# Performance work log

Hardware: AMD Instinct MI355X
Metric: run time of the kernel (lower is better)

The kernel has to match this reference:

```python
import jax, jax.numpy as jnp
import numpy as np
import math

B, S = 2, 2048                      # batch, seq_len (equal-length varlen pack)
NUM_HEADS, HEAD_DIM = 32, 128
NUM_KV_HEADS = 8                    # GQA group size = 4
WINDOW = 1024                       # sliding window (window_size, 0)
SCALE = 1.0 / math.sqrt(HEAD_DIM)


def get_slopes(n):
    # n=32 is a power of two -> simple geometric slopes (matches torch get_slopes)
    start = 2.0 ** (-2.0 ** (-(math.log2(n) - 3)))
    return np.array([start * start ** i for i in range(n)], dtype=np.float32)


def setup_inputs() -> dict:
    key = jax.random.key(0)
    kq, kk, kv = jax.random.split(key, 3)
    q = jax.random.normal(kq, (B * S, NUM_HEADS * HEAD_DIM), dtype=jnp.float32)
    k = jax.random.normal(kk, (B * S, NUM_KV_HEADS * HEAD_DIM), dtype=jnp.float32)
    v = jax.random.normal(kv, (B * S, NUM_KV_HEADS * HEAD_DIM), dtype=jnp.float32)
    return {"q": q, "k": k, "v": v}


def reference(q, k, v):
    # Prefill self-attention path of Attention.forward:
    # flash_attn_varlen_func(q, k, v, causal=True, window_size=(WINDOW, 0),
    #                        alibi_slopes=get_slopes(num_heads), softmax_scale=SCALE)
    slopes = jnp.asarray(get_slopes(NUM_HEADS))               # [H]
    qh = q.reshape(B, S, NUM_HEADS, HEAD_DIM)                 # [B,S,H,D]
    g = NUM_HEADS // NUM_KV_HEADS
    kh = jnp.repeat(k.reshape(B, S, NUM_KV_HEADS, HEAD_DIM), g, axis=2)
    vh = jnp.repeat(v.reshape(B, S, NUM_KV_HEADS, HEAD_DIM), g, axis=2)

    scores = jnp.einsum('bihd,bjhd->bhij', qh, kh) * SCALE    # [B,H,S,S]
    i = jnp.arange(S)[:, None]
    j = jnp.arange(S)[None, :]
    mask = (j <= i) & (j >= i - WINDOW)                       # causal + sliding window
    alibi = -slopes[:, None, None] * (i - j).astype(jnp.float32)  # [H,S,S]
    neg_inf = jnp.asarray(-jnp.inf, dtype=scores.dtype)
    scores = jnp.where(mask[None, None], scores + alibi[None], neg_inf)
    p = jax.nn.softmax(scores, axis=-1)
    o = jnp.einsum('bhij,bjhd->bihd', p, vh)                  # [B,S,H,D]
    return o.reshape(B * S, NUM_HEADS * HEAD_DIM)
```

## Files before the change

### kernel.cpp

```cpp
#include <hip/hip_runtime.h>
#include <stdint.h>

#define NB 2
#define NS 2048
#define NH 32
#define NKV 8
#define ND 128
#define NWIN 1024
#define KVB 32
#define SCALE2 (0.08838834764831845f * 1.4426950408889634f)
#define LOG2E 1.4426950408889634f

typedef __bf16 bf16x8 __attribute__((ext_vector_type(8)));
typedef float f32x4 __attribute__((ext_vector_type(4)));
typedef unsigned short u16x4 __attribute__((ext_vector_type(4)));
typedef unsigned short u16x8 __attribute__((ext_vector_type(8)));
typedef unsigned int u32x2 __attribute__((ext_vector_type(2)));

union Frag { u16x8 u; bf16x8 b; u32x2 w[2]; __bf16 e[8]; };
union BF4 { u16x4 u; __bf16 b[4]; };
union BF8 { u16x8 u; __bf16 b[8]; };

__device__ __forceinline__ void gload16(const unsigned short* g, unsigned short* l) {
  __builtin_amdgcn_global_load_lds(
      (const __attribute__((address_space(1))) unsigned int*)g,
      (__attribute__((address_space(3))) unsigned int*)l, 16, 0, 0);
}

__global__ __launch_bounds__(256)
void cvt_kv(const float* __restrict__ k, const float* __restrict__ v,
            unsigned short* __restrict__ kbf, unsigned short* __restrict__ vbf) {
  const int i = blockIdx.x * blockDim.x + threadIdx.x;
  float4 a0 = ((const float4*)k)[i * 2], a1 = ((const float4*)k)[i * 2 + 1];
  float4 b0 = ((const float4*)v)[i * 2], b1 = ((const float4*)v)[i * 2 + 1];
  BF8 ko, vo;
  ko.b[0] = (__bf16)a0.x; ko.b[1] = (__bf16)a0.y; ko.b[2] = (__bf16)a0.z; ko.b[3] = (__bf16)a0.w;
  ko.b[4] = (__bf16)a1.x; ko.b[5] = (__bf16)a1.y; ko.b[6] = (__bf16)a1.z; ko.b[7] = (__bf16)a1.w;
  vo.b[0] = (__bf16)b0.x; vo.b[1] = (__bf16)b0.y; vo.b[2] = (__bf16)b0.z; vo.b[3] = (__bf16)b0.w;
  vo.b[4] = (__bf16)b1.x; vo.b[5] = (__bf16)b1.y; vo.b[6] = (__bf16)b1.z; vo.b[7] = (__bf16)b1.w;
  ((u16x8*)kbf)[i] = ko.u;
  ((u16x8*)vbf)[i] = vo.u;
}

__global__ __launch_bounds__(256)
void attn_gqa(const unsigned short* __restrict__ kbf,
              const unsigned short* __restrict__ vbf,
              const float* __restrict__ qg, float* __restrict__ og) {
  __shared__ unsigned short k_lds[3][KVB * 128];
  __shared__ unsigned short v_lds[3][KVB * 128];

  const int tid = threadIdx.x;
  const int w = tid >> 6;
  const int lane = tid & 63;
  const int l15 = lane & 15;
  const int lg = lane >> 4;

  const int bid = blockIdx.x;
  const int hkv = bid & 7;
  const int rest = bid >> 3;
  const int b = (rest >= 48) ? 1 : 0;
  const int slot = rest - b * 48;
  const int h = hkv * 4 + w;
  const float slope2 = exp2f(-0.25f * (float)(h + 1)) * LOG2E;

  int koff_e[2], voff_e[2];
#pragma unroll
  for (int i = 0; i < 2; ++i) {
    const int rk = (w * 2 + i) * 4 + lg;
    const int c = l15;
    const int sig = ((rk >> 2) & 3) * 8 + ((rk >> 4) & 1) * 4 + (rk & 3);
    koff_e[i] = sig * (NKV * ND) + ((c ^ (rk & 7)) * 8);
    const int e0 = (w * 2 + i) * 512 + lane * 8;
    const int sx0 = e0 & 15;
    const int vj = (e0 >> 4) & 3;
    const int vg_ = (e0 >> 6) & 3;
    const int s1 = (e0 >> 8) & 1;
    const int scv = (e0 >> 9) & 7;
    voff_e[i] = (vg_ * 8 + s1 * 4 + vj) * (NKV * ND) + scv * 16 + sx0;
  }
  const unsigned short* kpan = kbf + (size_t)b * NS * (NKV * ND) + hkv * ND;
  const unsigned short* vpan = vbf + (size_t)b * NS * (NKV * ND) + hkv * ND;

  auto stage = [&](int t, int buf) {
    const size_t eb = (size_t)(t * KVB) * (NKV * ND);
#pragma unroll
    for (int i = 0; i < 2; ++i) {
      gload16(kpan + eb + koff_e[i], &k_lds[buf][(w * 2 + i) * 512]);
      gload16(vpan + eb + voff_e[i], &v_lds[buf][(w * 2 + i) * 512]);
    }
  };

  auto run_band = [&](int q0) {
    const int qiA = q0 + l15;
    const int qiB = qiA + 16;

    u16x8 qfA[4], qfB[4];
#pragma unroll
    for (int half = 0; half < 2; ++half) {
      const int qi = half ? qiB : qiA;
      const float* qp = qg + (size_t)(b * NS + qi) * (NH * ND) + h * ND;
#pragma unroll
      for (int ks = 0; ks < 4; ++ks) {
        const int dbase = ks * 32 + lg * 8;
        float4 f0 = *(const float4*)(qp + dbase);
        float4 f1 = *(const float4*)(qp + dbase + 4);
        Frag q_;
        q_.e[0] = (__bf16)f0.x; q_.e[1] = (__bf16)f0.y;
        q_.e[2] = (__bf16)f0.z; q_.e[3] = (__bf16)f0.w;
        q_.e[4] = (__bf16)f1.x; q_.e[5] = (__bf16)f1.y;
        q_.e[6] = (__bf16)f1.z; q_.e[7] = (__bf16)f1.w;
        if (half) qfB[ks] = q_.u; else qfA[ks] = q_.u;
      }
    }

    float mA = 0.f, lA = 0.f, mB = 0.f, lB = 0.f;
    f32x4 accA[8], accB[8];
#pragma unroll
    for (int c = 0; c < 8; ++c) {
      accA[c][0] = 0.f; accA[c][1] = 0.f; accA[c][2] = 0.f; accA[c][3] = 0.f;
      accB[c][0] = 0.f; accB[c][1] = 0.f; accB[c][2] = 0.f; accB[c][3] = 0.f;
    }

    const int t0 = (q0 >= NWIN) ? ((q0 - NWIN) >> 5) : 0;
    const int t1 = q0 >> 5;

    stage(t1, 0);
    if (t1 - 1 >= t0) stage(t1 - 1, 1);

    int idx = 0;
    for (int t = t1; t >= t0; --t, ++idx) {
      const int kvbase = t * KVB;
      if (t > t0) asm volatile("s_waitcnt vmcnt(4)" ::: "memory");
      else        asm volatile("s_waitcnt vmcnt(0)" ::: "memory");
      __builtin_amdgcn_s_barrier();
      if (t - 2 >= t0) stage(t - 2, (idx + 2) % 3);
      const int cur = idx % 3;

      const bool interior = (kvbase + 31 <= q0) && (kvbase >= q0 + 31 - NWIN);

      f32x4 sA[2], sB[2];
#pragma unroll
      for (int f = 0; f < 2; ++f) {
        sA[f][0] = 0.f; sA[f][1] = 0.f; sA[f][2] = 0.f; sA[f][3] = 0.f;
        sB[f][0] = 0.f; sB[f][1] = 0.f; sB[f][2] = 0.f; sB[f][3] = 0.f;
      }
      const int xo = (l15 & 7) << 4;
      __builtin_amdgcn_s_setprio(1);
#pragma unroll
      for (int ks = 0; ks < 4; ++ks) {
        const int db2 = ks * 64 + lg * 16;
        Frag qa, qb;
        qa.u = qfA[ks]; qb.u = qfB[ks];
#pragma unroll
        for (int f = 0; f < 2; ++f) {
          Frag kb;
          kb.u = *(const u16x8*)((const char*)&k_lds[cur][0] +
                                 (((f * 16 + l15) * 256 + db2) ^ xo));
          sA[f] = __builtin_amdgcn_mfma_f32_16x16x32_bf16(kb.b, qa.b, sA[f], 0, 0, 0);
          sB[f] = __builtin_amdgcn_mfma_f32_16x16x32_bf16(kb.b, qb.b, sB[f], 0, 0, 0);
        }
      }
      __builtin_amdgcn_s_setprio(0);

      Frag pbA, pbB;
      auto softmax_half = [&](const f32x4* s, int dbse, float& m_r, float& l_r,
                              f32x4* acc, Frag& pb) {
        float x[2][4];
        if (interior) {
          const float ab2 = fmaf(-slope2, (float)dbse, -m_r);
#pragma unroll
          for (int f = 0; f < 2; ++f)
#pragma unroll
            for (int r = 0; r < 4; ++r)
              x[f][r] = fmaf(s[f][r], SCALE2,
                             fmaf(slope2, (float)(f * 4 + r), ab2));
        } else {
#pragma unroll
          for (int f = 0; f < 2; ++f)
#pragma unroll
            for (int r = 0; r < 4; ++r) {
              const int d = dbse - (f * 4 + r);
              const float val = fmaf(s[f][r], SCALE2, -slope2 * (float)d) - m_r;
              x[f][r] = ((unsigned)d <= (unsigned)NWIN) ? val : -1e30f;
            }
        }
        float tm = fmaxf(fmaxf(fmaxf(x[0][0], x[0][1]), x[0][2]),
                         fmaxf(fmaxf(x[0][3], x[1][0]), x[1][1]));
        tm = fmaxf(tm, fmaxf(x[1][2], x[1][3]));
        if (!__all(tm <= 8.0f)) {
          tm = fmaxf(tm, __shfl_xor(tm, 16, 64));
          tm = fmaxf(tm, __shfl_xor(tm, 32, 64));
          const float delta = fmaxf(tm, 0.f);
          const float fac = __builtin_amdgcn_exp2f(-delta);
          m_r += delta;
          l_r *= fac;
#pragma unroll
          for (int c = 0; c < 8; ++c) acc[c] = acc[c] * fac;
#pragma unroll
          for (int f = 0; f < 2; ++f)
#pragma unroll
            for (int r = 0; r < 4; ++r) x[f][r] -= delta;
        }
        float e[8];
#pragma unroll
        for (int f = 0; f < 2; ++f)
#pragma unroll
          for (int r = 0; r < 4; ++r) {
            e[f * 4 + r] = __builtin_amdgcn_exp2f(x[f][r]);
            pb.e[f * 4 + r] = (__bf16)e[f * 4 + r];
          }
        l_r += ((e[0] + e[1]) + (e[2] + e[3])) + ((e[4] + e[5]) + (e[6] + e[7]));
      };
      softmax_half(sA, qiA - kvbase - lg * 8, mA, lA, accA, pbA);
      softmax_half(sB, qiB - kvbase - lg * 8, mB, lB, accB, pbB);

      Frag vb4[4];
      const unsigned int vbase = (unsigned int)(uintptr_t)(&v_lds[cur][0]) + lane * 8;
#pragma unroll
      for (int cp = 0; cp < 4; ++cp) {
        const unsigned int a = vbase + cp * 1024;
        asm volatile("ds_read_b64_tr_b16 %0, %1" : "=v"(vb4[cp].w[0]) : "v"(a));
        asm volatile("ds_read_b64_tr_b16 %0, %1 offset:512" : "=v"(vb4[cp].w[1]) : "v"(a));
      }
      __builtin_amdgcn_s_setprio(1);
#pragma unroll
      for (int c = 0; c < 8; ++c) {
        if (c == 5)      asm volatile("s_waitcnt lgkmcnt(4)" ::: "memory");
        else if (c == 6) asm volatile("s_waitcnt lgkmcnt(2)" ::: "memory");
        else if (c == 7) asm volatile("s_waitcnt lgkmcnt(0)" ::: "memory");
        else             asm volatile("s_waitcnt lgkmcnt(6)" ::: "memory");
        __builtin_amdgcn_sched_barrier(0);
        accA[c] = __builtin_amdgcn_mfma_f32_16x16x32_bf16(vb4[c & 3].b, pbA.b, accA[c], 0, 0, 0);
        accB[c] = __builtin_amdgcn_mfma_f32_16x16x32_bf16(vb4[c & 3].b, pbB.b, accB[c], 0, 0, 0);
        if (c < 4) {
          const unsigned int a2 = vbase + (c + 4) * 1024;
          asm volatile("ds_read_b64_tr_b16 %0, %1" : "=v"(vb4[c].w[0]) : "v"(a2));
          asm volatile("ds_read_b64_tr_b16 %0, %1 offset:512" : "=v"(vb4[c].w[1]) : "v"(a2));
        }
      }
      __builtin_amdgcn_s_setprio(0);
      __builtin_amdgcn_sched_barrier(0);
    }

    lA += __shfl_xor(lA, 16, 64);
    lA += __shfl_xor(lA, 32, 64);
    lB += __shfl_xor(lB, 16, 64);
    lB += __shfl_xor(lB, 32, 64);
    {
      const float inv = 1.0f / lA;
      float* op = og + (size_t)(b * NS + qiA) * (NH * ND) + h * ND + lg * 4;
#pragma unroll
      for (int c = 0; c < 8; ++c) { f32x4 o = accA[c] * inv; *(f32x4*)(op + c * 16) = o; }
    }
    {
      const float inv = 1.0f / lB;
      float* op = og + (size_t)(b * NS + qiB) * (NH * ND) + h * ND + lg * 4;
#pragma unroll
      for (int c = 0; c < 8; ++c) { f32x4 o = accB[c] * inv; *(f32x4*)(op + c * 16) = o; }
    }
    __builtin_amdgcn_s_barrier();
  };

  if (slot < 32) {
    run_band((slot + 32) * 32);
  } else {
    const int s = slot - 32;
    run_band(s * 32);
    run_band((31 - s) * 32);
  }
}

__global__ __launch_bounds__(256, 2)
void attn_fb(const float* __restrict__ qg, const float* __restrict__ kg,
             const float* __restrict__ vg, float* __restrict__ og) {
  __shared__ unsigned short k_lds[64 * 128];
  __shared__ unsigned short v_lds[64 * 128];
  const int tid = threadIdx.x;
  const int w = tid >> 6;
  const int lane = tid & 63;
  const int l15 = lane & 15;
  const int lg = lane >> 4;
  const int bid = blockIdx.x;
  const int h = bid & 31;
  const int qt = 31 - ((bid >> 5) & 31);
  const int b = bid >> 10;
  const int hkv = h >> 2;
  const float slope2 = exp2f(-0.25f * (float)(h + 1)) * LOG2E;
  const int q0 = qt * 64;
  const int qi = q0 + w * 16 + l15;
  u16x8 qf[4];
  {
    const float* qp = qg + (size_t)(b * NS + qi) * (NH * ND) + h * ND;
#pragma unroll
    for (int ks = 0; ks < 4; ++ks) {
      const int dbase = ks * 32 + lg * 8;
      float4 f0 = *(const float4*)(qp + dbase);
      float4 f1 = *(const float4*)(qp + dbase + 4);
      Frag q_;
      q_.e[0] = (__bf16)f0.x; q_.e[1] = (__bf16)f0.y;
      q_.e[2] = (__bf16)f0.z; q_.e[3] = (__bf16)f0.w;
      q_.e[4] = (__bf16)f1.x; q_.e[5] = (__bf16)f1.y;
      q_.e[6] = (__bf16)f1.z; q_.e[7] = (__bf16)f1.w;
      qf[ks] = q_.u;
    }
  }
  float m_r = -1e30f, l_r = 0.f;
  f32x4 acc[8];
#pragma unroll
  for (int c = 0; c < 8; ++c) { acc[c][0] = 0.f; acc[c][1] = 0.f; acc[c][2] = 0.f; acc[c][3] = 0.f; }
  const int srow = tid >> 5;
  const int sdb = (tid & 31) * 4;
  const int sc = sdb >> 4;
  const int sx = sdb & 15;
  float4 kreg[8], vreg[8];
  const int t0 = (q0 >= NWIN) ? ((q0 - NWIN) >> 6) : 0;
  const int t1 = q0 >> 6;
  auto load_tile = [&](int t) {
    const int kvbase = t * 64;
#pragma unroll
    for (int it = 0; it < 8; ++it) {
      const size_t go = (size_t)(b * NS + kvbase + it * 8 + srow) * (NKV * ND) + hkv * ND + sdb;
      kreg[it] = *(const float4*)(kg + go);
      vreg[it] = *(const float4*)(vg + go);
    }
  };
  load_tile(t0);
  for (int t = t0; t <= t1; ++t) {
    const int kvbase = t * 64;
    __syncthreads();
#pragma unroll
    for (int it = 0; it < 8; ++it) {
      const int row = it * 8 + srow;
      BF4 ku, vu;
      ku.b[0] = (__bf16)kreg[it].x; ku.b[1] = (__bf16)kreg[it].y;
      ku.b[2] = (__bf16)kreg[it].z; ku.b[3] = (__bf16)kreg[it].w;
      vu.b[0] = (__bf16)vreg[it].x; vu.b[1] = (__bf16)vreg[it].y;
      vu.b[2] = (__bf16)vreg[it].z; vu.b[3] = (__bf16)vreg[it].w;
      const int rk = ((row & 4) << 3) | ((row & 56) >> 1) | (row & 3);
      const int kb = (rk * 256 + sdb * 2) ^ ((rk & 7) << 4);
      *(u16x4*)((char*)k_lds + kb) = ku.u;
      const int s2 = ((row >> 5) << 1) | ((row >> 2) & 1);
      const int vi = sc * 1024 + s2 * 256 + ((row >> 3) & 3) * 64 + (row & 3) * 16 + sx;
      *(u16x4*)(&v_lds[vi]) = vu.u;
    }
    __syncthreads();
    if (t < t1) load_tile(t + 1);
    f32x4 s[4];
#pragma unroll
    for (int f = 0; f < 4; ++f) { s[f][0] = 0.f; s[f][1] = 0.f; s[f][2] = 0.f; s[f][3] = 0.f; }
    const int xo = (l15 & 7) << 4;
#pragma unroll
    for (int ks = 0; ks < 4; ++ks) {
      const int db2 = ks * 64 + lg * 16;
      Frag qa; qa.u = qf[ks];
#pragma unroll
      for (int f = 0; f < 4; ++f) {
        Frag kb;
        kb.u = *(u16x8*)((char*)k_lds + (((f * 16 + l15) * 256 + db2) ^ xo));
        s[f] = __builtin_amdgcn_mfma_f32_16x16x32_bf16(kb.b, qa.b, s[f], 0, 0, 0);
      }
    }
    const int dbse = qi - kvbase - lg * 8;
    float sv[4][4];
#pragma unroll
    for (int f = 0; f < 4; ++f) {
#pragma unroll
      for (int r = 0; r < 4; ++r) {
        const int koff = ((f & 1) << 5) + ((f >> 1) << 2) + r;
        const int d = dbse - koff;
        const float val = fmaf(s[f][r], SCALE2, -slope2 * (float)d);
        sv[f][r] = ((unsigned)d <= (unsigned)NWIN) ? val : -1e30f;
      }
    }
    float tm = fmaxf(fmaxf(sv[0][0], sv[0][1]), fmaxf(sv[0][2], sv[0][3]));
#pragma unroll
    for (int f = 1; f < 4; ++f)
      tm = fmaxf(tm, fmaxf(fmaxf(sv[f][0], sv[f][1]), fmaxf(sv[f][2], sv[f][3])));
    tm = fmaxf(tm, __shfl_xor(tm, 16, 64));
    tm = fmaxf(tm, __shfl_xor(tm, 32, 64));
    const float newm = fmaxf(m_r, tm);
    const float fac = __builtin_amdgcn_exp2f(m_r - newm);
    m_r = newm;
    float rs = 0.f;
    Frag pb0, pb1;
#pragma unroll
    for (int f = 0; f < 4; ++f) {
      float e0 = __builtin_amdgcn_exp2f(sv[f][0] - m_r);
      float e1 = __builtin_amdgcn_exp2f(sv[f][1] - m_r);
      float e2 = __builtin_amdgcn_exp2f(sv[f][2] - m_r);
      float e3 = __builtin_amdgcn_exp2f(sv[f][3] - m_r);
      rs += (e0 + e1) + (e2 + e3);
      const int base = (f >> 1) * 4;
      if (f & 1) {
        pb1.e[base + 0] = (__bf16)e0; pb1.e[base + 1] = (__bf16)e1;
        pb1.e[base + 2] = (__bf16)e2; pb1.e[base + 3] = (__bf16)e3;
      } else {
        pb0.e[base + 0] = (__bf16)e0; pb0.e[base + 1] = (__bf16)e1;
        pb0.e[base + 2] = (__bf16)e2; pb0.e[base + 3] = (__bf16)e3;
      }
    }
    rs += __shfl_xor(rs, 16, 64);
    rs += __shfl_xor(rs, 32, 64);
    l_r = l_r * fac + rs;
#pragma unroll
    for (int c = 0; c < 8; ++c) acc[c] = acc[c] * fac;
    const unsigned int vbase = (unsigned int)(uintptr_t)(&v_lds[0]) + lane * 8;
#pragma unroll
    for (int c = 0; c < 8; ++c) {
      u32x2 r0, r1, r2, r3;
      const unsigned int a = vbase + c * 2048;
      asm volatile("ds_read_b64_tr_b16 %0, %1" : "=v"(r0) : "v"(a));
      asm volatile("ds_read_b64_tr_b16 %0, %1 offset:512" : "=v"(r1) : "v"(a));
      asm volatile("ds_read_b64_tr_b16 %0, %1 offset:1024" : "=v"(r2) : "v"(a));
      asm volatile("ds_read_b64_tr_b16 %0, %1 offset:1536" : "=v"(r3) : "v"(a));
      asm volatile("s_waitcnt lgkmcnt(0)" ::: "memory");
      __builtin_amdgcn_sched_barrier(0);
      Frag vb0, vb1;
      vb0.w[0] = r0; vb0.w[1] = r1;
      vb1.w[0] = r2; vb1.w[1] = r3;
      acc[c] = __builtin_amdgcn_mfma_f32_16x16x32_bf16(vb0.b, pb0.b, acc[c], 0, 0, 0);
      acc[c] = __builtin_amdgcn_mfma_f32_16x16x32_bf16(vb1.b, pb1.b, acc[c], 0, 0, 0);
    }
  }
  const float inv = 1.0f / l_r;
  float* op = og + (size_t)(b * NS + qi) * (NH * ND) + h * ND + lg * 4;
#pragma unroll
  for (int c = 0; c < 8; ++c) { f32x4 o = acc[c] * inv; *(f32x4*)(op + c * 16) = o; }
}

extern "C" void kernel_launch(void* const* d_in, const int* in_sizes, int n_in,
                              void* d_out, int out_size, void* d_ws, size_t ws_size,
                              hipStream_t stream) {
  (void)in_sizes; (void)n_in; (void)out_size;
  const float* q = (const float*)d_in[0];
  const float* k = (const float*)d_in[1];
  const float* v = (const float*)d_in[2];
  float* out = (float*)d_out;
  const size_t kv_elems = (size_t)NB * NS * NKV * ND;
  const size_t need = 2 * kv_elems * sizeof(unsigned short);
  if (ws_size >= need) {
    unsigned short* kbf = (unsigned short*)d_ws;
    unsigned short* vbf = kbf + kv_elems;
    cvt_kv<<<dim3((unsigned)(kv_elems / 8 / 256)), dim3(256), 0, stream>>>(k, v, kbf, vbf);
    attn_gqa<<<dim3(NB * NKV * 48), dim3(256), 0, stream>>>(kbf, vbf, q, out);
  } else {
    attn_fb<<<dim3(NB * NH * (NS / 64)), dim3(256), 0, stream>>>(q, k, v, out);
  }
}
```

Measured before the change: 122.2 us.

## Replace LDS-staged GQA attention with direct-from-global loads and pre-transposed V

The LDS-staged, barrier-synchronised GQA kernel is replaced. In the old kernel four query heads shared a KV panel through a triple-buffered LDS pipeline. In the new one each wave handles one (batch, head, 32-query tile) independently and loads K and V fragments straight from global memory. A separate preprocessing kernel transposes V into a d-major bf16 layout so the PV MFMA operands can be read as contiguous 16-byte loads. This removes LDS traffic and barriers, at the cost of losing cross-head KV sharing and any async prefetch overlap, and adds an extra launch. The per-block work split also changes from paired causal bands to one wave per tile, with the largest tiles scheduled first.

New measurement: 218.7 us. 79.0% more time.

```diff
diff --git a/kernel.cpp b/kernel.cpp
--- a/kernel.cpp
+++ b/kernel.cpp
@@ -21,252 +21,219 @@
 union BF4 { u16x4 u; __bf16 b[4]; };
 union BF8 { u16x8 u; __bf16 b[8]; };
 
-__device__ __forceinline__ void gload16(const unsigned short* g, unsigned short* l) {
-  __builtin_amdgcn_global_load_lds(
-      (const __attribute__((address_space(1))) unsigned int*)g,
-      (__attribute__((address_space(3))) unsigned int*)l, 16, 0, 0);
+__device__ __forceinline__ unsigned short f2b(float x) {
+  union { __bf16 b; unsigned short u; } c; c.b = (__bf16)x; return c.u;
 }
 
 __global__ __launch_bounds__(256)
-void cvt_kv(const float* __restrict__ k, const float* __restrict__ v,
-            unsigned short* __restrict__ kbf, unsigned short* __restrict__ vbf) {
+void cvt_k(const float* __restrict__ k, unsigned short* __restrict__ kbf) {
   const int i = blockIdx.x * blockDim.x + threadIdx.x;
   float4 a0 = ((const float4*)k)[i * 2], a1 = ((const float4*)k)[i * 2 + 1];
-  float4 b0 = ((const float4*)v)[i * 2], b1 = ((const float4*)v)[i * 2 + 1];
-  BF8 ko, vo;
+  BF8 ko;
   ko.b[0] = (__bf16)a0.x; ko.b[1] = (__bf16)a0.y; ko.b[2] = (__bf16)a0.z; ko.b[3] = (__bf16)a0.w;
   ko.b[4] = (__bf16)a1.x; ko.b[5] = (__bf16)a1.y; ko.b[6] = (__bf16)a1.z; ko.b[7] = (__bf16)a1.w;
-  vo.b[0] = (__bf16)b0.x; vo.b[1] = (__bf16)b0.y; vo.b[2] = (__bf16)b0.z; vo.b[3] = (__bf16)b0.w;
-  vo.b[4] = (__bf16)b1.x; vo.b[5] = (__bf16)b1.y; vo.b[6] = (__bf16)b1.z; vo.b[7] = (__bf16)b1.w;
   ((u16x8*)kbf)[i] = ko.u;
-  ((u16x8*)vbf)[i] = vo.u;
 }
 
 __global__ __launch_bounds__(256)
-void attn_gqa(const unsigned short* __restrict__ kbf,
-              const unsigned short* __restrict__ vbf,
-              const float* __restrict__ qg, float* __restrict__ og) {
-  __shared__ unsigned short k_lds[3][KVB * 128];
-  __shared__ unsigned short v_lds[3][KVB * 128];
-
+void vt_cvt(const float* __restrict__ v, unsigned short* __restrict__ vt) {
+  __shared__ unsigned short lt[128][72];
+  const int bid = blockIdx.x;
+  const int kt = bid & 31;
+  const int hkv = (bid >> 5) & 7;
+  const int b = bid >> 8;
+  const int t = threadIdx.x;
+  const int r = t >> 2;
+  const int dc = (t & 3) * 32;
+  const float* src = v + (size_t)(b * NS + kt * 64 + r) * (NKV * ND) + hkv * ND + dc;
+#pragma unroll
+  for (int j = 0; j < 8; ++j) {
+    float4 x = *(const float4*)(src + j * 4);
+    lt[dc + j * 4 + 0][r] = f2b(x.x);
+    lt[dc + j * 4 + 1][r] = f2b(x.y);
+    lt[dc + j * 4 + 2][r] = f2b(x.z);
+    lt[dc + j * 4 + 3][r] = f2b(x.w);
+  }
+  __syncthreads();
+  const int d = t >> 1;
+  const int kc = (t & 1) * 32;
+  unsigned short* dst = vt + (size_t)((b * NKV + hkv) * ND + d) * NS + kt * 64 + kc;
+#pragma unroll
+  for (int j2 = 0; j2 < 4; ++j2) {
+    u16x8 o;
+#pragma unroll
+    for (int e = 0; e < 8; ++e) o[e] = lt[d][kc + j2 * 8 + e];
+    *(u16x8*)(dst + j2 * 8) = o;
+  }
+}
+
+__global__ __launch_bounds__(256)
+void attn_nl(const unsigned short* __restrict__ kbf,
+             const unsigned short* __restrict__ vt,
+             const float* __restrict__ qg, float* __restrict__ og) {
   const int tid = threadIdx.x;
   const int w = tid >> 6;
   const int lane = tid & 63;
   const int l15 = lane & 15;
   const int lg = lane >> 4;
 
-  const int bid = blockIdx.x;
-  const int hkv = bid & 7;
-  const int rest = bid >> 3;
-  const int b = (rest >= 48) ? 1 : 0;
-  const int slot = rest - b * 48;
-  const int h = hkv * 4 + w;
+  const int u = blockIdx.x * 4 + w;
+  const int qt = 63 - (u >> 6);
+  const int hb = u & 63;
+  const int b = hb >> 5;
+  const int h = hb & 31;
+  const int hkv = h >> 2;
   const float slope2 = exp2f(-0.25f * (float)(h + 1)) * LOG2E;
-
-  int koff_e[2], voff_e[2];
-#pragma unroll
-  for (int i = 0; i < 2; ++i) {
-    const int rk = (w * 2 + i) * 4 + lg;
-    const int c = l15;
-    const int sig = ((rk >> 2) & 3) * 8 + ((rk >> 4) & 1) * 4 + (rk & 3);
-    koff_e[i] = sig * (NKV * ND) + ((c ^ (rk & 7)) * 8);
-    const int e0 = (w * 2 + i) * 512 + lane * 8;
-    const int sx0 = e0 & 15;
-    const int vj = (e0 >> 4) & 3;
-    const int vg_ = (e0 >> 6) & 3;
-    const int s1 = (e0 >> 8) & 1;
-    const int scv = (e0 >> 9) & 7;
-    voff_e[i] = (vg_ * 8 + s1 * 4 + vj) * (NKV * ND) + scv * 16 + sx0;
-  }
+  const int q0 = qt * 32;
+  const int qiA = q0 + l15;
+  const int qiB = qiA + 16;
+
+  u16x8 qfA[4], qfB[4];
+#pragma unroll
+  for (int half = 0; half < 2; ++half) {
+    const int qi = half ? qiB : qiA;
+    const float* qp = qg + (size_t)(b * NS + qi) * (NH * ND) + h * ND;
+#pragma unroll
+    for (int ks = 0; ks < 4; ++ks) {
+      const int dbase = ks * 32 + lg * 8;
+      float4 f0 = *(const float4*)(qp + dbase);
+      float4 f1 = *(const float4*)(qp + dbase + 4);
+      Frag q_;
+      q_.e[0] = (__bf16)f0.x; q_.e[1] = (__bf16)f0.y;
+      q_.e[2] = (__bf16)f0.z; q_.e[3] = (__bf16)f0.w;
+      q_.e[4] = (__bf16)f1.x; q_.e[5] = (__bf16)f1.y;
+      q_.e[6] = (__bf16)f1.z; q_.e[7] = (__bf16)f1.w;
+      if (half) qfB[ks] = q_.u; else qfA[ks] = q_.u;
+    }
+  }
+
   const unsigned short* kpan = kbf + (size_t)b * NS * (NKV * ND) + hkv * ND;
-  const unsigned short* vpan = vbf + (size_t)b * NS * (NKV * ND) + hkv * ND;
-
-  auto stage = [&](int t, int buf) {
-    const size_t eb = (size_t)(t * KVB) * (NKV * ND);
-#pragma unroll
-    for (int i = 0; i < 2; ++i) {
-      gload16(kpan + eb + koff_e[i], &k_lds[buf][(w * 2 + i) * 512]);
-      gload16(vpan + eb + voff_e[i], &v_lds[buf][(w * 2 + i) * 512]);
-    }
-  };
-
-  auto run_band = [&](int q0) {
-    const int qiA = q0 + l15;
-    const int qiB = qiA + 16;
-
-    u16x8 qfA[4], qfB[4];
-#pragma unroll
-    for (int half = 0; half < 2; ++half) {
-      const int qi = half ? qiB : qiA;
-      const float* qp = qg + (size_t)(b * NS + qi) * (NH * ND) + h * ND;
-#pragma unroll
-      for (int ks = 0; ks < 4; ++ks) {
-        const int dbase = ks * 32 + lg * 8;
-        float4 f0 = *(const float4*)(qp + dbase);
-        float4 f1 = *(const float4*)(qp + dbase + 4);
-        Frag q_;
-        q_.e[0] = (__bf16)f0.x; q_.e[1] = (__bf16)f0.y;
-        q_.e[2] = (__bf16)f0.z; q_.e[3] = (__bf16)f0.w;
-        q_.e[4] = (__bf16)f1.x; q_.e[5] = (__bf16)f1.y;
-        q_.e[6] = (__bf16)f1.z; q_.e[7] = (__bf16)f1.w;
-        if (half) qfB[ks] = q_.u; else qfA[ks] = q_.u;
+  const unsigned short* vpan = vt + (size_t)(b * NKV + hkv) * ND * NS;
+  const int sig0 = ((l15 >> 2) << 3) + (l15 & 3);
+
+  float mA = 0.f, lA = 0.f, mB = 0.f, lB = 0.f;
+  f32x4 accA[8], accB[8];
+#pragma unroll
+  for (int c = 0; c < 8; ++c) {
+    accA[c][0] = 0.f; accA[c][1] = 0.f; accA[c][2] = 0.f; accA[c][3] = 0.f;
+    accB[c][0] = 0.f; accB[c][1] = 0.f; accB[c][2] = 0.f; accB[c][3] = 0.f;
+  }
+
+  const int t0 = (q0 >= NWIN) ? ((q0 - NWIN) >> 5) : 0;
+  const int t1 = q0 >> 5;
+
+  for (int t = t1; t >= t0; --t) {
+    const int kvbase = t * KVB;
+    const bool interior = (kvbase + 31 <= q0) && (kvbase >= q0 + 31 - NWIN);
+
+    const unsigned short* k0 = kpan + (size_t)(kvbase + sig0) * (NKV * ND) + lg * 8;
+    const unsigned short* k1 = k0 + 4 * (NKV * ND);
+    Frag kf0[4], kf1[4];
+#pragma unroll
+    for (int ks = 0; ks < 4; ++ks) {
+      kf0[ks].u = *(const u16x8*)(k0 + ks * 32);
+      kf1[ks].u = *(const u16x8*)(k1 + ks * 32);
+    }
+
+    f32x4 sA[2], sB[2];
+#pragma unroll
+    for (int f = 0; f < 2; ++f) {
+      sA[f][0] = 0.f; sA[f][1] = 0.f; sA[f][2] = 0.f; sA[f][3] = 0.f;
+      sB[f][0] = 0.f; sB[f][1] = 0.f; sB[f][2] = 0.f; sB[f][3] = 0.f;
+    }
+    __builtin_amdgcn_s_setprio(1);
+#pragma unroll
+    for (int ks = 0; ks < 4; ++ks) {
+      Frag qa, qb;
+      qa.u = qfA[ks]; qb.u = qfB[ks];
+      sA[0] = __builtin_amdgcn_mfma_f32_16x16x32_bf16(kf0[ks].b, qa.b, sA[0], 0, 0, 0);
+      sB[0] = __builtin_amdgcn_mfma_f32_16x16x32_bf16(kf0[ks].b, qb.b, sB[0], 0, 0, 0);
+      sA[1] = __builtin_amdgcn_mfma_f32_16x16x32_bf16(kf1[ks].b, qa.b, sA[1], 0, 0, 0);
+      sB[1] = __builtin_amdgcn_mfma_f32_16x16x32_bf16(kf1[ks].b, qb.b, sB[1], 0, 0, 0);
+    }
+    __builtin_amdgcn_s_setprio(0);
+
+    Frag vf[8];
+#pragma unroll
+    for (int c = 0; c < 8; ++c)
+      vf[c].u = *(const u16x8*)(vpan + (size_t)(c * 16 + l15) * NS + kvbase + lg * 8);
+
+    Frag pbA, pbB;
+    auto softmax_half = [&](const f32x4* s, int dbse, float& m_r, float& l_r,
+                            f32x4* acc, Frag& pb) {
+      float x[2][4];
+      if (interior) {
+        const float ab2 = fmaf(-slope2, (float)dbse, -m_r);
+#pragma unroll
+        for (int f = 0; f < 2; ++f)
+#pragma unroll
+          for (int r = 0; r < 4; ++r)
+            x[f][r] = fmaf(s[f][r], SCALE2,
+                           fmaf(slope2, (float)(f * 4 + r), ab2));
+      } else {
+#pragma unroll
+        for (int f = 0; f < 2; ++f)
+#pragma unroll
+          for (int r = 0; r < 4; ++r) {
+            const int d = dbse - (f * 4 + r);
+            const float val = fmaf(s[f][r], SCALE2, -slope2 * (float)d) - m_r;
+            x[f][r] = ((unsigned)d <= (unsigned)NWIN) ? val : -1e30f;
+          }
       }
-    }
-
-    float mA = 0.f, lA = 0.f, mB = 0.f, lB = 0.f;
-    f32x4 accA[8], accB[8];
+      float tm = fmaxf(fmaxf(fmaxf(x[0][0], x[0][1]), x[0][2]),
+                       fmaxf(fmaxf(x[0][3], x[1][0]), x[1][1]));
+      tm = fmaxf(tm, fmaxf(x[1][2], x[1][3]));
+      if (!__all(tm <= 8.0f)) {
+        tm = fmaxf(tm, __shfl_xor(tm, 16, 64));
+        tm = fmaxf(tm, __shfl_xor(tm, 32, 64));
+        const float delta = fmaxf(tm, 0.f);
+        const float fac = __builtin_amdgcn_exp2f(-delta);
+        m_r += delta;
+        l_r *= fac;
+#pragma unroll
+        for (int c = 0; c < 8; ++c) acc[c] = acc[c] * fac;
+#pragma unroll
+        for (int f = 0; f < 2; ++f)
+#pragma unroll
+          for (int r = 0; r < 4; ++r) x[f][r] -= delta;
+      }
+      float e[8];
+#pragma unroll
+      for (int f = 0; f < 2; ++f)
+#pragma unroll
+        for (int r = 0; r < 4; ++r) {
+          e[f * 4 + r] = __builtin_amdgcn_exp2f(x[f][r]);
+          pb.e[f * 4 + r] = (__bf16)e[f * 4 + r];
+        }
+      l_r += ((e[0] + e[1]) + (e[2] + e[3])) + ((e[4] + e[5]) + (e[6] + e[7]));
+    };
+    softmax_half(sA, qiA - kvbase - lg * 8, mA, lA, accA, pbA);
+    softmax_half(sB, qiB - kvbase - lg * 8, mB, lB, accB, pbB);
+
+    __builtin_amdgcn_s_setprio(1);
 #pragma unroll
     for (int c = 0; c < 8; ++c) {
-      accA[c][0] = 0.f; accA[c][1] = 0.f; accA[c][2] = 0.f; accA[c][3] = 0.f;
-      accB[c][0] = 0.f; accB[c][1] = 0.f; accB[c][2] = 0.f; accB[c][3] = 0.f;
-    }
-
-    const int t0 = (q0 >= NWIN) ? ((q0 - NWIN) >> 5) : 0;
-    const int t1 = q0 >> 5;
-
-    stage(t1, 0);
-    if (t1 - 1 >= t0) stage(t1 - 1, 1);
-
-    int idx = 0;
-    for (int t = t1; t >= t0; --t, ++idx) {
-      const int kvbase = t * KVB;
-      if (t > t0) asm volatile("s_waitcnt vmcnt(4)" ::: "memory");
-      else        asm volatile("s_waitcnt vmcnt(0)" ::: "memory");
-      __builtin_amdgcn_s_barrier();
-      if (t - 2 >= t0) stage(t - 2, (idx + 2) % 3);
-      const int cur = idx % 3;
-
-      const bool interior = (kvbase + 31 <= q0) && (kvbase >= q0 + 31 - NWIN);
-
-      f32x4 sA[2], sB[2];
-#pragma unroll
-      for (int f = 0; f < 2; ++f) {
-        sA[f][0] = 0.f; sA[f][1] = 0.f; sA[f][2] = 0.f; sA[f][3] = 0.f;
-        sB[f][0] = 0.f; sB[f][1] = 0.f; sB[f][2] = 0.f; sB[f][3] = 0.f;
-      }
-      const int xo = (l15 & 7) << 4;
-      __builtin_amdgcn_s_setprio(1);
-#pragma unroll
-      for (int ks = 0; ks < 4; ++ks) {
-        const int db2 = ks * 64 + lg * 16;
-        Frag qa, qb;
-        qa.u = qfA[ks]; qb.u = qfB[ks];
-#pragma unroll
-        for (int f = 0; f < 2; ++f) {
-          Frag kb;
-          kb.u = *(const u16x8*)((const char*)&k_lds[cur][0] +
-                                 (((f * 16 + l15) * 256 + db2) ^ xo));
-          sA[f] = __builtin_amdgcn_mfma_f32_16x16x32_bf16(kb.b, qa.b, sA[f], 0, 0, 0);
-          sB[f] = __builtin_amdgcn_mfma_f32_16x16x32_bf16(kb.b, qb.b, sB[f], 0, 0, 0);
-        }
-      }
-      __builtin_amdgcn_s_setprio(0);
-
-      Frag pbA, pbB;
-      auto softmax_half = [&](const f32x4* s, int dbse, float& m_r, float& l_r,
-                              f32x4* acc, Frag& pb) {
-        float x[2][4];
-        if (interior) {
-          const float ab2 = fmaf(-slope2, (float)dbse, -m_r);
-#pragma unroll
-          for (int f = 0; f < 2; ++f)
-#pragma unroll
-            for (int r = 0; r < 4; ++r)
-              x[f][r] = fmaf(s[f][r], SCALE2,
-                             fmaf(slope2, (float)(f * 4 + r), ab2));
-        } else {
-#pragma unroll
-          for (int f = 0; f < 2; ++f)
-#pragma unroll
-            for (int r = 0; r < 4; ++r) {
-              const int d = dbse - (f * 4 + r);
-              const float val = fmaf(s[f][r], SCALE2, -slope2 * (float)d) - m_r;
-              x[f][r] = ((unsigned)d <= (unsigned)NWIN) ? val : -1e30f;
-            }
-        }
-        float tm = fmaxf(fmaxf(fmaxf(x[0][0], x[0][1]), x[0][2]),
-                         fmaxf(fmaxf(x[0][3], x[1][0]), x[1][1]));
-        tm = fmaxf(tm, fmaxf(x[1][2], x[1][3]));
-        if (!__all(tm <= 8.0f)) {
-          tm = fmaxf(tm, __shfl_xor(tm, 16, 64));
-          tm = fmaxf(tm, __shfl_xor(tm, 32, 64));
-          const float delta = fmaxf(tm, 0.f);
-          const float fac = __builtin_amdgcn_exp2f(-delta);
-          m_r += delta;
-          l_r *= fac;
-#pragma unroll
-          for (int c = 0; c < 8; ++c) acc[c] = acc[c] * fac;
-#pragma unroll
-          for (int f = 0; f < 2; ++f)
-#pragma unroll
-            for (int r = 0; r < 4; ++r) x[f][r] -= delta;
-        }
-        float e[8];
-#pragma unroll
-        for (int f = 0; f < 2; ++f)
-#pragma unroll
-          for (int r = 0; r < 4; ++r) {
-            e[f * 4 + r] = __builtin_amdgcn_exp2f(x[f][r]);
-            pb.e[f * 4 + r] = (__bf16)e[f * 4 + r];
-          }
-        l_r += ((e[0] + e[1]) + (e[2] + e[3])) + ((e[4] + e[5]) + (e[6] + e[7]));
-      };
-      softmax_half(sA, qiA - kvbase - lg * 8, mA, lA, accA, pbA);
-      softmax_half(sB, qiB - kvbase - lg * 8, mB, lB, accB, pbB);
-
-      Frag vb4[4];
-      const unsigned int vbase = (unsigned int)(uintptr_t)(&v_lds[cur][0]) + lane * 8;
-#pragma unroll
-      for (int cp = 0; cp < 4; ++cp) {
-        const unsigned int a = vbase + cp * 1024;
-        asm volatile("ds_read_b64_tr_b16 %0, %1" : "=v"(vb4[cp].w[0]) : "v"(a));
-        asm volatile("ds_read_b64_tr_b16 %0, %1 offset:512" : "=v"(vb4[cp].w[1]) : "v"(a));
-      }
-      __builtin_amdgcn_s_setprio(1);
-#pragma unroll
-      for (int c = 0; c < 8; ++c) {
-        if (c == 5)      asm volatile("s_waitcnt lgkmcnt(4)" ::: "memory");
-        else if (c == 6) asm volatile("s_waitcnt lgkmcnt(2)" ::: "memory");
-        else if (c == 7) asm volatile("s_waitcnt lgkmcnt(0)" ::: "memory");
-        else             asm volatile("s_waitcnt lgkmcnt(6)" ::: "memory");
-        __builtin_amdgcn_sched_barrier(0);
-        accA[c] = __builtin_amdgcn_mfma_f32_16x16x32_bf16(vb4[c & 3].b, pbA.b, accA[c], 0, 0, 0);
-        accB[c] = __builtin_amdgcn_mfma_f32_16x16x32_bf16(vb4[c & 3].b, pbB.b, accB[c], 0, 0, 0);
-        if (c < 4) {
-          const unsigned int a2 = vbase + (c + 4) * 1024;
-          asm volatile("ds_read_b64_tr_b16 %0, %1" : "=v"(vb4[c].w[0]) : "v"(a2));
-          asm volatile("ds_read_b64_tr_b16 %0, %1 offset:512" : "=v"(vb4[c].w[1]) : "v"(a2));
-        }
-      }
-      __builtin_amdgcn_s_setprio(0);
-      __builtin_amdgcn_sched_barrier(0);
-    }
-
-    lA += __shfl_xor(lA, 16, 64);
-    lA += __shfl_xor(lA, 32, 64);
-    lB += __shfl_xor(lB, 16, 64);
-    lB += __shfl_xor(lB, 32, 64);
-    {
-      const float inv = 1.0f / lA;
-      float* op = og + (size_t)(b * NS + qiA) * (NH * ND) + h * ND + lg * 4;
-#pragma unroll
-      for (int c = 0; c < 8; ++c) { f32x4 o = accA[c] * inv; *(f32x4*)(op + c * 16) = o; }
-    }
-    {
-      const float inv = 1.0f / lB;
-      float* op = og + (size_t)(b * NS + qiB) * (NH * ND) + h * ND + lg * 4;
-#pragma unroll
-      for (int c = 0; c < 8; ++c) { f32x4 o = accB[c] * inv; *(f32x4*)(op + c * 16) = o; }
-    }
-    __builtin_amdgcn_s_barrier();
-  };
-
-  if (slot < 32) {
-    run_band((slot + 32) * 32);
-  } else {
-    const int s = slot - 32;
-    run_band(s * 32);
-    run_band((31 - s) * 32);
+      accA[c] = __builtin_amdgcn_mfma_f32_16x16x32_bf16(vf[c].b, pbA.b, accA[c], 0, 0, 0);
+      accB[c] = __builtin_amdgcn_mfma_f32_16x16x32_bf16(vf[c].b, pbB.b, accB[c], 0, 0, 0);
+    }
+    __builtin_amdgcn_s_setprio(0);
+  }
+
+  lA += __shfl_xor(lA, 16, 64);
+  lA += __shfl_xor(lA, 32, 64);
+  lB += __shfl_xor(lB, 16, 64);
+  lB += __shfl_xor(lB, 32, 64);
+  {
+    const float inv = 1.0f / lA;
+    float* op = og + (size_t)(b * NS + qiA) * (NH * ND) + h * ND + lg * 4;
+#pragma unroll
+    for (int c = 0; c < 8; ++c) { f32x4 o = accA[c] * inv; *(f32x4*)(op + c * 16) = o; }
+  }
+  {
+    const float inv = 1.0f / lB;
+    float* op = og + (size_t)(b * NS + qiB) * (NH * ND) + h * ND + lg * 4;
+#pragma unroll
+    for (int c = 0; c < 8; ++c) { f32x4 o = accB[c] * inv; *(f32x4*)(op + c * 16) = o; }
   }
 }
 
@@ -440,9 +407,10 @@
   const size_t need = 2 * kv_elems * sizeof(unsigned short);
   if (ws_size >= need) {
     unsigned short* kbf = (unsigned short*)d_ws;
-    unsigned short* vbf = kbf + kv_elems;
-    cvt_kv<<<dim3((unsigned)(kv_elems / 8 / 256)), dim3(256), 0, stream>>>(k, v, kbf, vbf);
-    attn_gqa<<<dim3(NB * NKV * 48), dim3(256), 0, stream>>>(kbf, vbf, q, out);
+    unsigned short* vtp = kbf + kv_elems;
+    cvt_k<<<dim3((unsigned)(kv_elems / 8 / 256)), dim3(256), 0, stream>>>(k, kbf);
+    vt_cvt<<<dim3(NB * NKV * (NS / 64)), dim3(256), 0, stream>>>(v, vtp);
+    attn_nl<<<dim3(1024), dim3(256), 0, stream>>>(kbf, vtp, q, out);
   } else {
     attn_fb<<<dim3(NB * NH * (NS / 64)), dim3(256), 0, stream>>>(q, k, v, out);
   }
```
